# Kernel optimization log

Hardware: AMD Instinct MI355X
Metric: run time of the kernel (lower is better)

The kernel has to match this reference:

```python
import jax, jax.numpy as jnp
import numpy as np

D_MODEL = 1024
NUM_HEADS = 16
HEAD_DIM = D_MODEL // NUM_HEADS
D_FF = 4096
B, S = 4, 2048
EPS = 1e-5


def layernorm(x, gamma, beta):
    mu = jnp.mean(x, axis=-1, keepdims=True)
    var = jnp.mean(jnp.square(x - mu), axis=-1, keepdims=True)
    return (x - mu) * jax.lax.rsqrt(var + EPS) * gamma + beta


def setup_inputs() -> dict:
    key = jax.random.key(0)
    ks = jax.random.split(key, 16)
    s_in = 1.0 / np.sqrt(D_MODEL)
    s_ff = 1.0 / np.sqrt(D_FF)
    return {
        "x": jax.random.normal(ks[0], (B, S, D_MODEL), jnp.float32),
        "Wq": jax.random.normal(ks[1], (D_MODEL, D_MODEL), jnp.float32) * s_in,
        "bq": jnp.zeros((D_MODEL,), jnp.float32),
        "Wk": jax.random.normal(ks[2], (D_MODEL, D_MODEL), jnp.float32) * s_in,
        "bk": jnp.zeros((D_MODEL,), jnp.float32),
        "Wv": jax.random.normal(ks[3], (D_MODEL, D_MODEL), jnp.float32) * s_in,
        "bv": jnp.zeros((D_MODEL,), jnp.float32),
        "Wo": jax.random.normal(ks[4], (D_MODEL, D_MODEL), jnp.float32) * s_in,
        "bo": jnp.zeros((D_MODEL,), jnp.float32),
        "W1": jax.random.normal(ks[5], (D_MODEL, D_FF), jnp.float32) * s_in,
        "b1": jnp.zeros((D_FF,), jnp.float32),
        "W2": jax.random.normal(ks[6], (D_FF, D_MODEL), jnp.float32) * s_ff,
        "b2": jnp.zeros((D_MODEL,), jnp.float32),
        "g1": jnp.ones((D_MODEL,), jnp.float32),
        "be1": jnp.zeros((D_MODEL,), jnp.float32),
        "g2": jnp.ones((D_MODEL,), jnp.float32),
        "be2": jnp.zeros((D_MODEL,), jnp.float32),
    }


def reference(x, Wq, bq, Wk, bk, Wv, bv, Wo, bo, W1, b1, W2, b2, g1, be1, g2, be2):
    # multi-head self-attention (dropout is identity at eval)
    def split_heads(t):  # [B,S,D] -> [B,H,S,hd]
        return t.reshape(B, S, NUM_HEADS, HEAD_DIM).transpose(0, 2, 1, 3)

    q = split_heads(x @ Wq + bq)
    k = split_heads(x @ Wk + bk)
    v = split_heads(x @ Wv + bv)
    scores = jnp.einsum("bhqd,bhkd->bhqk", q, k) / np.sqrt(HEAD_DIM)
    attn = jax.nn.softmax(scores, axis=-1)
    out = jnp.einsum("bhqk,bhkd->bhqd", attn, v)
    out = out.transpose(0, 2, 1, 3).reshape(B, S, D_MODEL)
    attn_out = out @ Wo + bo

    h = layernorm(x + attn_out, g1, be1)
    ff = jax.nn.relu(h @ W1 + b1) @ W2 + b2
    return layernorm(h + ff, g2, be2)
```

## Files before the change

### kernel.cpp

```cpp
#include <hip/hip_runtime.h>
#include <hip/hip_bf16.h>


#define DM    1024
#define DFF   4096
#define NH    16
#define HD    64
#define BATCH 4
#define SEQ   2048
#define TOK   (BATCH * SEQ)

typedef __attribute__((ext_vector_type(8))) __bf16 bf16x8;
typedef __attribute__((ext_vector_type(4))) float f32x4;
typedef __attribute__((ext_vector_type(16))) float f32x16;
typedef __attribute__((ext_vector_type(4))) unsigned short u16x4;

typedef const __attribute__((address_space(1))) unsigned int* gas1_t;
typedef __attribute__((address_space(3))) unsigned int* las3_t;

__device__ __forceinline__ void gl_lds16(const void* g, void* l) {
  __builtin_amdgcn_global_load_lds((gas1_t)g, (las3_t)l, 16, 0, 0);
}

__device__ __forceinline__ unsigned short f2bu(float x) {
  return __builtin_bit_cast(unsigned short, __float2bfloat16(x));
}

__device__ __forceinline__ unsigned pk_bf16_trunc(float hi, float lo) {
  return __builtin_amdgcn_perm(__builtin_bit_cast(unsigned, hi),
                               __builtin_bit_cast(unsigned, lo), 0x07060302u);
}

__global__ __launch_bounds__(256) void cast_bf16(
    const float* __restrict__ in, unsigned short* __restrict__ out, int n4) {
  int i = blockIdx.x * 256 + threadIdx.x;
  if (i >= n4) return;
  float4 v = ((const float4*)in)[i];
  u16x4 o = {f2bu(v.x), f2bu(v.y), f2bu(v.z), f2bu(v.w)};
  ((u16x4*)out)[i] = o;
}

__global__ __launch_bounds__(256) void transpose_cast(
    const float* __restrict__ in, unsigned short* __restrict__ out, int K, int N) {
  __shared__ float tile[32][33];
  int n0 = blockIdx.x * 32, k0 = blockIdx.y * 32;
  int tx = threadIdx.x, ty = threadIdx.y;
#pragma unroll
  for (int i = 0; i < 4; ++i)
    tile[ty + 8 * i][tx] = in[(size_t)(k0 + ty + 8 * i) * N + n0 + tx];
  __syncthreads();
#pragma unroll
  for (int i = 0; i < 4; ++i)
    out[(size_t)(n0 + ty + 8 * i) * K + k0 + tx] = f2bu(tile[tx][ty + 8 * i]);
}

__global__ __launch_bounds__(256) void transpose_cast4(
    const float* __restrict__ A0, const float* __restrict__ A1,
    const float* __restrict__ A2, const float* __restrict__ A3,
    unsigned short* __restrict__ O0, unsigned short* __restrict__ O1,
    unsigned short* __restrict__ O2, unsigned short* __restrict__ O3) {
  __shared__ float tile[32][33];
  const float* in; unsigned short* out;
  switch (blockIdx.z) {
    case 0: in = A0; out = O0; break;
    case 1: in = A1; out = O1; break;
    case 2: in = A2; out = O2; break;
    default: in = A3; out = O3; break;
  }
  int n0 = blockIdx.x * 32, k0 = blockIdx.y * 32;
  int tx = threadIdx.x, ty = threadIdx.y;
#pragma unroll
  for (int i = 0; i < 4; ++i)
    tile[ty + 8 * i][tx] = in[(size_t)(k0 + ty + 8 * i) * DM + n0 + tx];
  __syncthreads();
#pragma unroll
  for (int i = 0; i < 4; ++i)
    out[(size_t)(n0 + ty + 8 * i) * DM + k0 + tx] = f2bu(tile[tx][ty + 8 * i]);
}

__device__ __forceinline__ void mma8(const bf16x8 a0, const bf16x8 a1,
                                     const bf16x8 b, f32x16* c0, f32x16* c1) {
  *c0 = __builtin_amdgcn_mfma_f32_32x32x16_bf16(a0, b, *c0, 0, 0, 0);
  *c1 = __builtin_amdgcn_mfma_f32_32x32x16_bf16(a1, b, *c1, 0, 0, 0);
}

__device__ __forceinline__ void mainloop256(
    const unsigned short* __restrict__ A, int lda,
    const unsigned short* __restrict__ Bt, int ldb, int Kl,
    int m0, int n0, unsigned short* As, unsigned short* Bs,
    f32x16 acc[2][2][2]) {
  const int tid = threadIdx.x, lane = tid & 63, w = tid >> 6;
  const int l31 = lane & 31, khalf = lane >> 5;
  const int wr = w >> 2, wc = w & 3;
  const int rA0 = wr * 64 + l31, rA1 = rA0 + 32, rB = wc * 32 + l31;

  const unsigned short* pa[2][2];
  const unsigned short* pb[2][2];
#pragma unroll
  for (int h = 0; h < 2; ++h)
#pragma unroll
    for (int i = 0; i < 2; ++i) {
      const int g = (i * 8 + w) * 64 + lane;
      const int r = g >> 3;
      const int cs = ((g & 7) ^ (r & 7)) * 8;
      pa[h][i] = A + (size_t)(m0 + h * 128 + r) * lda + cs;
      pb[h][i] = Bt + (size_t)(n0 + h * 128 + r) * ldb + cs;
    }
  const int wofsB = w * 1024;

  bf16x8 aF[2][4], b0[4], b1[4];

#define STA(BUF, H, I) \
  gl_lds16(pa[H][I], (char*)As + (BUF) * 32768 + (H) * 16384 + (I) * 8192 + wofsB)
#define STB(BUF, H, I) \
  gl_lds16(pb[H][I], (char*)Bs + (BUF) * 32768 + (H) * 16384 + (I) * 8192 + wofsB)
#define ADV_A(H) { pa[H][0] += 64; pa[H][1] += 64; }
#define ADV_B(H) { pb[H][0] += 64; pb[H][1] += 64; }

#define RD_A(BUFB, H)                                                         \
  { const char* Ah = (const char*)As + (BUFB) + (H) * 16384;                  \
    _Pragma("unroll") for (int ks = 0; ks < 4; ++ks) {                        \
      const int c = ks * 2 + khalf;                                           \
      aF[0][ks] = *(const bf16x8*)(Ah + rA0 * 128 + ((c ^ (rA0 & 7)) << 4));  \
      aF[1][ks] = *(const bf16x8*)(Ah + rA1 * 128 + ((c ^ (rA1 & 7)) << 4));  \
    } }
#define RD_B(DST, BUFB, H)                                                    \
  { const char* Bh = (const char*)Bs + (BUFB) + (H) * 16384;                  \
    _Pragma("unroll") for (int ks = 0; ks < 4; ++ks) {                        \
      const int c = ks * 2 + khalf;                                           \
      DST[ks] = *(const bf16x8*)(Bh + rB * 128 + ((c ^ (rB & 7)) << 4));      \
    } }

#define MMA4(QM, QN, BV)                                                      \
  { __builtin_amdgcn_s_setprio(1);                                           \
    _Pragma("unroll") for (int ks = 0; ks < 4; ++ks)                          \
      mma8(aF[0][ks], aF[1][ks], BV[ks], &acc[QM][QN][0], &acc[QM][QN][1]);   \
    __builtin_amdgcn_s_setprio(0); }

#define TILE(BUF, STG, W0, W1, W3)                                            \
  RD_A((BUF) * 32768, 0);                                                     \
  RD_B(b0, (BUF) * 32768, 0);                                                 \
  if (STG) { STA((BUF) ^ 1, 0, 0); STA((BUF) ^ 1, 0, 1); ADV_A(0);            \
             STB((BUF) ^ 1, 0, 0); STB((BUF) ^ 1, 0, 1); ADV_B(0); }          \
  asm volatile(W0 "\n\ts_barrier" ::: "memory");                              \
  MMA4(0, 0, b0);                                                             \
  RD_B(b1, (BUF) * 32768, 1);                                                 \
  if (STG) { STB((BUF) ^ 1, 1, 0); STB((BUF) ^ 1, 1, 1); ADV_B(1); }          \
  asm volatile(W1 "\n\ts_barrier" ::: "memory");                              \
  MMA4(0, 1, b1);                                                             \
  RD_A((BUF) * 32768, 1);                                                     \
  if (STG) { STA((BUF) ^ 1, 1, 0); STA((BUF) ^ 1, 1, 1); ADV_A(1); }          \
  MMA4(1, 1, b1);                                                             \
  RD_B(b0, (BUF) * 32768, 0);                                                 \
  asm volatile(W3 "\n\ts_barrier" ::: "memory");                              \
  MMA4(1, 0, b0);

  STA(0, 0, 0); STA(0, 0, 1); STB(0, 0, 0); STB(0, 0, 1);
  STB(0, 1, 0); STB(0, 1, 1); STA(0, 1, 0); STA(0, 1, 1);
  ADV_A(0); ADV_B(0); ADV_B(1); ADV_A(1);
  asm volatile("s_waitcnt vmcnt(4)\n\ts_barrier" ::: "memory");

  const int NT = Kl >> 6;
  for (int t = 0; t + 2 < NT; t += 2) {
    TILE(0, 1, "s_waitcnt vmcnt(6)", "s_waitcnt vmcnt(6)", "s_waitcnt vmcnt(4)");
    TILE(1, 1, "s_waitcnt vmcnt(6)", "s_waitcnt vmcnt(6)", "s_waitcnt vmcnt(4)");
  }
  TILE(0, 1, "s_waitcnt vmcnt(6)", "s_waitcnt vmcnt(6)", "s_waitcnt vmcnt(4)");
  TILE(1, 0, "s_waitcnt vmcnt(2)", "s_waitcnt vmcnt(0)", "");

#undef TILE
#undef MMA4
#undef RD_B
#undef RD_A
#undef ADV_B
#undef ADV_A
#undef STB
#undef STA
}


__device__ __forceinline__ void xcd_swizzle(int& bx, int& by) {
  const int gx = gridDim.x, nxy = gx * gridDim.y;
  int lin = by * gx + bx;
  lin = (lin & 7) * (nxy >> 3) + (lin >> 3);
  bx = lin % gx;
  by = lin / gx;
}

__global__ __launch_bounds__(512, 2) void gemm256(
    const unsigned short* __restrict__ A, int lda,
    const unsigned short* __restrict__ Bt, int ldb, int Kl,
    const float* __restrict__ bias, void* __restrict__ C0,
    void* __restrict__ C1, int N, float alpha, int relu, int ofp32) {
  __shared__ unsigned short As[32768];
  __shared__ unsigned short Bs[32768];
  const int tid = threadIdx.x, lane = tid & 63, w = tid >> 6;
  const int l31 = lane & 31, khalf = lane >> 5;
  const int wr = w >> 2, wc = w & 3;
  int bx = blockIdx.x, by = blockIdx.y;
  xcd_swizzle(bx, by);
  const int m0 = by * 256, n0 = bx * 256;
  const int koff = blockIdx.z * Kl;
  void* Cout = blockIdx.z ? C1 : C0;
  const float* be = blockIdx.z ? nullptr : bias;

  f32x16 acc[2][2][2];
#pragma unroll
  for (int qm = 0; qm < 2; ++qm)
#pragma unroll
    for (int qn = 0; qn < 2; ++qn)
#pragma unroll
      for (int mi = 0; mi < 2; ++mi)
#pragma unroll
        for (int r = 0; r < 16; ++r) acc[qm][qn][mi][r] = 0.f;

  mainloop256(A + koff, lda, Bt + koff, ldb, Kl, m0, n0, As, Bs, acc);

#pragma unroll
  for (int qn = 0; qn < 2; ++qn) {
    const int col = n0 + qn * 128 + wc * 32 + l31;
    const float bvv = be ? be[col] : 0.f;
#pragma unroll
    for (int qm = 0; qm < 2; ++qm)
#pragma unroll
      for (int mi = 0; mi < 2; ++mi) {
#pragma unroll
        for (int g = 0; g < 4; ++g) {
          const int rbase = m0 + qm * 128 + wr * 64 + mi * 32 + g * 8 + khalf * 4;
#pragma unroll
          for (int r = 0; r < 4; ++r) {
            float val = alpha * (acc[qm][qn][mi][g * 4 + r] + bvv);
            if (relu) val = fmaxf(val, 0.f);
            size_t idx = (size_t)(rbase + r) * N + col;
            if (ofp32) ((float*)Cout)[idx] = val;
            else ((unsigned short*)Cout)[idx] = f2bu(val);
          }
        }
      }
  }
}

#define QSCALE 0.18033688f

__global__ __launch_bounds__(512, 2) void gemm_qkv256(
    const unsigned short* __restrict__ A, const unsigned short* __restrict__ Bt,
    const float* __restrict__ bq, const float* __restrict__ bk,
    const float* __restrict__ bv,
    unsigned short* __restrict__ Qb, unsigned short* __restrict__ Kb,
    unsigned short* __restrict__ Vtg) {
  __shared__ unsigned short As[32768];
  __shared__ unsigned short Bs[32768];
  const int tid = threadIdx.x, lane = tid & 63, w = tid >> 6;
  const int l31 = lane & 31, khalf = lane >> 5;
  const int wr = w >> 2, wc = w & 3;
  int bx = blockIdx.x, by = blockIdx.y;
  xcd_swizzle(bx, by);
  const int m0 = by * 256, n0 = bx * 256;

  f32x16 acc[2][2][2];
#pragma unroll
  for (int qm = 0; qm < 2; ++qm)
#pragma unroll
    for (int qn = 0; qn < 2; ++qn)
#pragma unroll
      for (int mi = 0; mi < 2; ++mi)
#pragma unroll
        for (int r = 0; r < 16; ++r) acc[qm][qn][mi][r] = 0.f;

  mainloop256(A, DM, Bt, DM, DM, m0, n0, As, Bs, acc);

  const int region = n0 >> 10;
  if (region < 2) {
    unsigned short* Out = region ? Kb : Qb;
    const float* bias = region ? bk : bq;
    const float alpha = region ? 1.0f : QSCALE;
#pragma unroll
    for (int qn = 0; qn < 2; ++qn) {
      const int col = (n0 & 1023) + qn * 128 + wc * 32 + l31;
      const float bvv = bias[col];
#pragma unroll
      for (int qm = 0; qm < 2; ++qm)
#pragma unroll
        for (int mi = 0; mi < 2; ++mi) {
#pragma unroll
          for (int g = 0; g < 4; ++g) {
            const int rbase = m0 + qm * 128 + wr * 64 + mi * 32 + g * 8 + khalf * 4;
#pragma unroll
            for (int r = 0; r < 4; ++r)
              Out[(size_t)(rbase + r) * DM + col] =
                  f2bu(alpha * (acc[qm][qn][mi][g * 4 + r] + bvv));
          }
        }
    }
  } else {
#pragma unroll
    for (int qn = 0; qn < 2; ++qn) {
      const int col = (n0 & 1023) + qn * 128 + wc * 32 + l31;
      const float bvv = bv[col];
      const int hh = col >> 6, dl = col & 63;
#pragma unroll
      for (int qm = 0; qm < 2; ++qm)
#pragma unroll
        for (int mi = 0; mi < 2; ++mi) {
#pragma unroll
          for (int g = 0; g < 4; ++g) {
            const int sbase = m0 + qm * 128 + wr * 64 + mi * 32 + g * 8 + khalf * 4;
            const int b_ = sbase >> 11, s0 = sbase & 2047;
            u16x4 pk;
#pragma unroll
            for (int r = 0; r < 4; ++r)
              pk[r] = f2bu(acc[qm][qn][mi][g * 4 + r] + bvv);
            *(u16x4*)(Vtg + ((size_t)((b_ * NH + hh) * HD + dl)) * SEQ + s0) = pk;
          }
        }
    }
  }
}

__global__ __launch_bounds__(256) void attn_kernel(
    const unsigned short* __restrict__ Q, const unsigned short* __restrict__ K,
    const unsigned short* __restrict__ Vtg, unsigned short* __restrict__ O) {
  __shared__ unsigned short Kt[4][64 * 64];
  __shared__ unsigned short Vt[4][64 * 64];
  __shared__ unsigned short Pt[4][32 * 64];

  const int tid = threadIdx.x, lane = tid & 63, w = tid >> 6;
  const int l15 = lane & 15, quad = lane >> 4;
  const int q0 = blockIdx.x * 128;
  const int bh = blockIdx.y, b = bh >> 4, hh = bh & 15;
  const size_t tokbase = (size_t)b * SEQ;

  bf16x8 qf[2][2];
#pragma unroll
  for (int qg = 0; qg < 2; ++qg)
#pragma unroll
    for (int kk = 0; kk < 2; ++kk)
      qf[qg][kk] = *(const bf16x8*)(Q +
          (tokbase + q0 + w * 32 + qg * 16 + l15) * DM + hh * HD + kk * 32 + quad * 8);

  float l_run[2] = {0.f, 0.f};
  f32x4 Oacc[2][4];
#pragma unroll
  for (int qg = 0; qg < 2; ++qg)
#pragma unroll
    for (int nt = 0; nt < 4; ++nt) Oacc[qg][nt] = {0.f, 0.f, 0.f, 0.f};

  char* ptw = (char*)&Pt[w][0];

  int rowS[2], csrcS[2];
#pragma unroll
  for (int i = 0; i < 2; ++i) {
    int f = (i * 4 + w) * 64 + lane;
    rowS[i] = f >> 3;
    csrcS[i] = ((f & 7) ^ (rowS[i] & 7)) * 8;
  }
  const unsigned short* kg[2];
  const unsigned short* vg[2];
#pragma unroll
  for (int i = 0; i < 2; ++i) {
    kg[i] = K + (tokbase + rowS[i]) * DM + hh * HD + csrcS[i];
    vg[i] = Vtg + ((size_t)bh * HD + rowS[i]) * SEQ + csrcS[i];
  }

#define STAGE_KV(BUF)                                                         \
  { _Pragma("unroll") for (int i = 0; i < 2; ++i) {                           \
      gl_lds16(kg[i], (char*)Kt + (BUF) * 8192 + (i * 4 + w) * 1024);         \
      gl_lds16(vg[i], (char*)Vt + (BUF) * 8192 + (i * 4 + w) * 1024);         \
      kg[i] += 64 * DM;                                                       \
      vg[i] += 64;                                                            \
    } }

  const int NT = SEQ / 64;
  STAGE_KV(0);
  STAGE_KV(1);

  for (int j = 0; j < NT; ++j) {
    const int buf = j & 3;
    if (j + 2 < NT) STAGE_KV((j + 2) & 3);
    if (j < NT - 2)
      asm volatile("s_waitcnt vmcnt(8)\n\ts_barrier" ::: "memory");
    else if (j == NT - 2)
      asm volatile("s_waitcnt vmcnt(4)\n\ts_barrier" ::: "memory");
    else
      asm volatile("s_waitcnt vmcnt(0)\n\ts_barrier" ::: "memory");

    const char* ktb = (const char*)Kt + buf * 8192;
    const char* vtb = (const char*)Vt + buf * 8192;

    f32x4 S[2][4];
#pragma unroll
    for (int qg = 0; qg < 2; ++qg)
#pragma unroll
      for (int mt = 0; mt < 4; ++mt) S[qg][mt] = {0.f, 0.f, 0.f, 0.f};
#pragma unroll
    for (int kk = 0; kk < 2; ++kk) {
#pragma unroll
      for (int mt = 0; mt < 4; ++mt) {
        bf16x8 aK = *(const bf16x8*)(ktb + (mt * 16 + l15) * 128 +
                                     (((kk * 4 + quad) ^ (l15 & 7)) * 16));
        S[0][mt] = __builtin_amdgcn_mfma_f32_16x16x32_bf16(aK, qf[0][kk], S[0][mt], 0, 0, 0);
        S[1][mt] = __builtin_amdgcn_mfma_f32_16x16x32_bf16(aK, qf[1][kk], S[1][mt], 0, 0, 0);
      }
    }

#pragma unroll
    for (int qg = 0; qg < 2; ++qg) {
      float rs = 0.f;
#pragma unroll
      for (int mt = 0; mt < 4; ++mt) {
        float p0 = __builtin_amdgcn_exp2f(S[qg][mt][0]);
        float p1 = __builtin_amdgcn_exp2f(S[qg][mt][1]);
        float p2 = __builtin_amdgcn_exp2f(S[qg][mt][2]);
        float p3 = __builtin_amdgcn_exp2f(S[qg][mt][3]);
        rs += (p0 + p1) + (p2 + p3);
        uint2 pk = {pk_bf16_trunc(p1, p0), pk_bf16_trunc(p3, p2)};
        *(uint2*)(ptw + (qg * 16 + l15) * 128 +
                  (((mt * 2 + (quad >> 1)) ^ (l15 & 7)) * 16 + (quad & 1) * 8)) = pk;
      }
      l_run[qg] += rs;
    }

#pragma unroll
    for (int kk = 0; kk < 2; ++kk) {
      bf16x8 aP[2];
#pragma unroll
      for (int qg = 0; qg < 2; ++qg)
        aP[qg] = *(const bf16x8*)(ptw + (qg * 16 + l15) * 128 +
                                  (((kk * 4 + quad) ^ (l15 & 7)) * 16));
#pragma unroll
      for (int nt = 0; nt < 4; ++nt) {
        bf16x8 bV = *(const bf16x8*)(vtb + (nt * 16 + l15) * 128 +
                                     (((kk * 4 + quad) ^ (l15 & 7)) * 16));
        Oacc[0][nt] = __builtin_amdgcn_mfma_f32_16x16x32_bf16(aP[0], bV, Oacc[0][nt], 0, 0, 0);
        Oacc[1][nt] = __builtin_amdgcn_mfma_f32_16x16x32_bf16(aP[1], bV, Oacc[1][nt], 0, 0, 0);
      }
    }
  }
#undef STAGE_KV

#pragma unroll
  for (int qg = 0; qg < 2; ++qg) {
    l_run[qg] += __shfl_xor(l_run[qg], 16);
    l_run[qg] += __shfl_xor(l_run[qg], 32);
  }
#pragma unroll
  for (int qg = 0; qg < 2; ++qg) {
    f32x4 li;
#pragma unroll
    for (int r = 0; r < 4; ++r) li[r] = 1.0f / __shfl(l_run[qg], quad * 4 + r);
#pragma unroll
    for (int nt = 0; nt < 4; ++nt)
#pragma unroll
      for (int r = 0; r < 4; ++r) {
        size_t tok = tokbase + q0 + w * 32 + qg * 16 + quad * 4 + r;
        O[tok * DM + hh * HD + nt * 16 + l15] = f2bu(Oacc[qg][nt][r] * li[r]);
      }
  }
}

__global__ __launch_bounds__(256) void ln_res(
    const float* __restrict__ base, const float* __restrict__ d0,
    const float* __restrict__ d1,
    const float* __restrict__ gamma, const float* __restrict__ beta,
    float* __restrict__ outf, unsigned short* __restrict__ outb) {
  __shared__ float red[8];
  const int row = blockIdx.x, tid = threadIdx.x;
  const size_t rb = (size_t)row * DM;
  float4 xv = ((const float4*)(base + rb))[tid];
  float4 dv = ((const float4*)(d0 + rb))[tid];
  float s0 = xv.x + dv.x, s1 = xv.y + dv.y, s2 = xv.z + dv.z, s3 = xv.w + dv.w;
  if (d1) {
    float4 ev = ((const float4*)(d1 + rb))[tid];
    s0 += ev.x; s1 += ev.y; s2 += ev.z; s3 += ev.w;
  }
  float t = s0 + s1 + s2 + s3;
#pragma unroll
  for (int m = 1; m < 64; m <<= 1) t += __shfl_xor(t, m);
  if ((tid & 63) == 0) red[tid >> 6] = t;
  __syncthreads();
  float mu = (red[0] + red[1] + red[2] + red[3]) * (1.0f / DM);
  float dd0 = s0 - mu, dd1 = s1 - mu, dd2 = s2 - mu, dd3 = s3 - mu;
  float v = dd0 * dd0 + dd1 * dd1 + dd2 * dd2 + dd3 * dd3;
#pragma unroll
  for (int m = 1; m < 64; m <<= 1) v += __shfl_xor(v, m);
  if ((tid & 63) == 0) red[4 + (tid >> 6)] = v;
  __syncthreads();
  float var = (red[4] + red[5] + red[6] + red[7]) * (1.0f / DM);
  float rs = rsqrtf(var + 1e-5f);
  float4 gv = ((const float4*)gamma)[tid];
  float4 bv = ((const float4*)beta)[tid];
  float o0 = dd0 * rs * gv.x + bv.x;
  float o1 = dd1 * rs * gv.y + bv.y;
  float o2 = dd2 * rs * gv.z + bv.z;
  float o3 = dd3 * rs * gv.w + bv.w;
  float4 ov = {o0, o1, o2, o3};
  ((float4*)(outf + rb))[tid] = ov;
  if (outb) {
    u16x4 ob = {f2bu(o0), f2bu(o1), f2bu(o2), f2bu(o3)};
    ((u16x4*)(outb + rb))[tid] = ob;
  }
}

extern "C" void kernel_launch(void* const* d_in, const int* in_sizes, int n_in,
                              void* d_out, int out_size, void* d_ws, size_t ws_size,
                              hipStream_t stream) {
  const float* x   = (const float*)d_in[0];
  const float* Wq  = (const float*)d_in[1];  const float* bq  = (const float*)d_in[2];
  const float* Wk  = (const float*)d_in[3];  const float* bk  = (const float*)d_in[4];
  const float* Wv  = (const float*)d_in[5];  const float* bvv = (const float*)d_in[6];
  const float* Wo  = (const float*)d_in[7];  const float* bo  = (const float*)d_in[8];
  const float* W1  = (const float*)d_in[9];  const float* b1  = (const float*)d_in[10];
  const float* W2  = (const float*)d_in[11]; const float* b2  = (const float*)d_in[12];
  const float* g1  = (const float*)d_in[13]; const float* be1 = (const float*)d_in[14];
  const float* g2  = (const float*)d_in[15]; const float* be2 = (const float*)d_in[16];

  char* ws = (char*)d_ws;
  const size_t MB = 1ull << 20;
  unsigned short* xb    = (unsigned short*)(ws + 0 * MB);
  unsigned short* wqkvT = (unsigned short*)(ws + 16 * MB);
  unsigned short* woT   = (unsigned short*)(ws + 22 * MB);
  unsigned short* w1T   = (unsigned short*)(ws + 24 * MB);
  unsigned short* w2T   = (unsigned short*)(ws + 32 * MB);
  unsigned short* Qb    = (unsigned short*)(ws + 40 * MB);
  unsigned short* Kb    = (unsigned short*)(ws + 56 * MB);
  unsigned short* Vtg   = (unsigned short*)(ws + 72 * MB);
  unsigned short* aO    = (unsigned short*)(ws + 104 * MB);
  float*          prj   = (float*)(ws + 120 * MB);
  float*          prj2  = (float*)(ws + 40 * MB);
  float*          h     = (float*)(ws + 152 * MB);
  unsigned short* hb    = (unsigned short*)(ws + 0 * MB);
  unsigned short* ffm   = (unsigned short*)(ws + 40 * MB);
  float*          ffo   = (float*)(ws + 104 * MB);
  float*          ffo2  = (float*)(ws + 0 * MB);
  (void)ws_size; (void)in_sizes; (void)n_in; (void)out_size;

  cast_bf16<<<TOK * DM / 4 / 256, 256, 0, stream>>>(x, xb, TOK * DM / 4);
  transpose_cast4<<<dim3(DM / 32, DM / 32, 4), dim3(32, 8), 0, stream>>>(
      Wq, Wk, Wv, Wo, wqkvT, wqkvT + 1024 * 1024, wqkvT + 2048 * 1024, woT);
  transpose_cast<<<dim3(DFF / 32, DM / 32), dim3(32, 8), 0, stream>>>(W1, w1T, DM, DFF);
  transpose_cast<<<dim3(DM / 32, DFF / 32), dim3(32, 8), 0, stream>>>(W2, w2T, DFF, DM);

  gemm_qkv256<<<dim3(3 * DM / 256, TOK / 256), 512, 0, stream>>>(
      xb, wqkvT, bq, bk, bvv, Qb, Kb, Vtg);

  attn_kernel<<<dim3(SEQ / 128, BATCH * NH), 256, 0, stream>>>(Qb, Kb, Vtg, aO);

  gemm256<<<dim3(DM / 256, TOK / 256, 2), 512, 0, stream>>>(
      aO, DM, woT, DM, DM / 2, bo, prj, prj2, DM, 1.0f, 0, 1);
  ln_res<<<TOK, 256, 0, stream>>>(x, prj, prj2, g1, be1, h, hb);

  gemm256<<<dim3(DFF / 256, TOK / 256, 1), 512, 0, stream>>>(
      hb, DM, w1T, DM, DM, b1, ffm, nullptr, DFF, 1.0f, 1, 0);
  gemm256<<<dim3(DM / 256, TOK / 256, 2), 512, 0, stream>>>(
      ffm, DFF, w2T, DFF, DFF / 2, b2, ffo, ffo2, DM, 1.0f, 0, 1);

  ln_res<<<TOK, 256, 0, stream>>>(h, ffo, ffo2, g2, be2, (float*)d_out, nullptr);
}
```

Measured before the change: 590.8 us.

## Restructure GEMM main loop into finer-grained staged pipeline with deeper prefetch

Replaces the two-tile TILE macro loop with an ITER body covering two K-tiles. Global-to-LDS loads for the quarter-tiles of the next buffer are issued further ahead and interleaved between each MMA quadrant, with barriers around every MMA group. The prologue now preloads one and a half tiles. The aim is to hide global load latency better and keep the matrix units fed. The cost is many more s_barrier instructions per iteration, plus the risk of LDS read/write hazards if the buffer-reuse order is wrong.

```diff
diff --git a/kernel.cpp b/kernel.cpp
--- a/kernel.cpp
+++ b/kernel.cpp
@@ -137,38 +137,58 @@
       mma8(aF[0][ks], aF[1][ks], BV[ks], &acc[QM][QN][0], &acc[QM][QN][1]);   \
     __builtin_amdgcn_s_setprio(0); }
 
-#define TILE(BUF, STG, W0, W1, W3)                                            \
-  RD_A((BUF) * 32768, 0);                                                     \
-  RD_B(b0, (BUF) * 32768, 0);                                                 \
-  if (STG) { STA((BUF) ^ 1, 0, 0); STA((BUF) ^ 1, 0, 1); ADV_A(0);            \
-             STB((BUF) ^ 1, 0, 0); STB((BUF) ^ 1, 0, 1); ADV_B(0); }          \
-  asm volatile(W0 "\n\ts_barrier" ::: "memory");                              \
-  MMA4(0, 0, b0);                                                             \
-  RD_B(b1, (BUF) * 32768, 1);                                                 \
-  if (STG) { STB((BUF) ^ 1, 1, 0); STB((BUF) ^ 1, 1, 1); ADV_B(1); }          \
-  asm volatile(W1 "\n\ts_barrier" ::: "memory");                              \
-  MMA4(0, 1, b1);                                                             \
-  RD_A((BUF) * 32768, 1);                                                     \
-  if (STG) { STA((BUF) ^ 1, 1, 0); STA((BUF) ^ 1, 1, 1); ADV_A(1); }          \
-  MMA4(1, 1, b1);                                                             \
-  RD_B(b0, (BUF) * 32768, 0);                                                 \
-  asm volatile(W3 "\n\ts_barrier" ::: "memory");                              \
-  MMA4(1, 0, b0);
-
-  STA(0, 0, 0); STA(0, 0, 1); STB(0, 0, 0); STB(0, 0, 1);
-  STB(0, 1, 0); STB(0, 1, 1); STA(0, 1, 0); STA(0, 1, 1);
-  ADV_A(0); ADV_B(0); ADV_B(1); ADV_A(1);
+#define BAR asm volatile("s_barrier" ::: "memory")
+
+#define ITER(SL, G3, G7)                                                      \
+                                                         \
+  RD_A(0, 0); RD_B(b0, 0, 0);                                                 \
+  STA(1, 1, 0); STA(1, 1, 1); ADV_A(1);                                       \
+  BAR; MMA4(0, 0, b0); BAR;                                                   \
+                                                         \
+  RD_B(b1, 0, 1);                                                             \
+  STB(1, 0, 0); STB(1, 0, 1); ADV_B(0);                                       \
+  BAR; MMA4(0, 1, b1); BAR;                                                   \
+                                                         \
+  RD_A(0, 1);                                                                 \
+  if (SL) { STA(0, 0, 0); STA(0, 0, 1); ADV_A(0); }                           \
+  BAR; MMA4(1, 1, b1); BAR;                                                   \
+                                    \
+  if (SL) { STB(0, 1, 0); STB(0, 1, 1); ADV_B(1); }                           \
+  asm volatile(G3 ::: "memory");                                              \
+  MMA4(1, 0, b0); BAR;                                                        \
+                                                         \
+  RD_A(32768, 0); RD_B(b0, 32768, 0);                                         \
+  if (SL) { STA(0, 1, 0); STA(0, 1, 1); ADV_A(1); }                           \
+  BAR; MMA4(0, 0, b0); BAR;                                                   \
+                                                         \
+  RD_B(b1, 32768, 1);                                                         \
+  if (SL) { STB(0, 0, 0); STB(0, 0, 1); ADV_B(0); }                           \
+  BAR; MMA4(0, 1, b1); BAR;                                                   \
+                                                         \
+  RD_A(32768, 1);                                                             \
+  if (SL) { STA(1, 0, 0); STA(1, 0, 1); ADV_A(0); }                           \
+  BAR; MMA4(1, 1, b1); BAR;                                                   \
+                        \
+  if (SL) { STB(1, 1, 0); STB(1, 1, 1); ADV_B(1); }                           \
+  asm volatile(G7 ::: "memory");                                              \
+  MMA4(1, 0, b0); BAR;
+
+  STA(0, 0, 0); STA(0, 0, 1); ADV_A(0);
+  STB(0, 0, 0); STB(0, 0, 1); ADV_B(0);
+  STB(0, 1, 0); STB(0, 1, 1); ADV_B(1);
+  STA(0, 1, 0); STA(0, 1, 1); ADV_A(1);
+  STA(1, 0, 0); STA(1, 0, 1); ADV_A(0);
+  STB(1, 1, 0); STB(1, 1, 1); ADV_B(1);
   asm volatile("s_waitcnt vmcnt(4)\n\ts_barrier" ::: "memory");
 
-  const int NT = Kl >> 6;
-  for (int t = 0; t + 2 < NT; t += 2) {
-    TILE(0, 1, "s_waitcnt vmcnt(6)", "s_waitcnt vmcnt(6)", "s_waitcnt vmcnt(4)");
-    TILE(1, 1, "s_waitcnt vmcnt(6)", "s_waitcnt vmcnt(6)", "s_waitcnt vmcnt(4)");
-  }
-  TILE(0, 1, "s_waitcnt vmcnt(6)", "s_waitcnt vmcnt(6)", "s_waitcnt vmcnt(4)");
-  TILE(1, 0, "s_waitcnt vmcnt(2)", "s_waitcnt vmcnt(0)", "");
-
-#undef TILE
+  const int L = (Kl >> 6) >> 1;
+  for (int i = 0; i < L - 1; ++i) {
+    ITER(1, "s_waitcnt vmcnt(4)\n\ts_barrier", "s_waitcnt vmcnt(4)\n\ts_barrier");
+  }
+  ITER(0, "s_waitcnt vmcnt(0)\n\ts_barrier", "s_barrier");
+
+#undef ITER
+#undef BAR
 #undef MMA4
 #undef RD_B
 #undef RD_A
```

Result: no change. 584.8 us (-1.0%).
